# Performance work log

Hardware: AMD Instinct MI355X
Metric: run time of the kernel (lower is better)

Reference implementation:

```python
import jax, jax.numpy as jnp
import numpy as np

N, D = 8192, 256

def setup_inputs() -> dict:
    key = jax.random.key(0)
    k1, k2 = jax.random.split(key)
    data = jnp.zeros((1,), dtype=jnp.float32)  # unused by the module
    Z = jax.random.normal(k1, (N, D), dtype=jnp.float32)
    A_hat = jax.random.uniform(k2, (N, N), dtype=jnp.float32)
    return {"data": data, "Z": Z, "A_hat": A_hat}

def reference(data, Z, A_hat):
    A = A_hat.astype(jnp.float32)
    # D^{-1/2} A D^{-1/2}: diagonal matmuls are mathematically row/col scaling
    d_inv_sqrt = 1.0 / jnp.sqrt(A.sum(axis=1) + 1e-10)  # [N]
    A_norm = A * d_inv_sqrt[:, None] * d_inv_sqrt[None, :]  # [N, N]
    # cosine similarity (F.normalize uses eps=1e-12 clamp on the norm)
    z_norm = jnp.linalg.norm(Z, axis=1, keepdims=True)
    Z_n = Z / jnp.maximum(z_norm, 1e-12)
    similarity = Z_n @ Z_n.T  # [N, N]
    homo_loss = -jnp.sum(A_norm * similarity)
    hetero_loss = jnp.sum((1.0 - A_norm) * similarity)
    return (homo_loss, hetero_loss)
```

## Files before the change

kernel.cpp:

```cpp
#include <hip/hip_runtime.h>
#include <hip/hip_fp16.h>

typedef _Float16 f16x8  __attribute__((ext_vector_type(8)));
typedef _Float16 f16x4  __attribute__((ext_vector_type(4)));
typedef float    f32x16 __attribute__((ext_vector_type(16)));

constexpr int Nn = 8192;
constexpr int Dd = 256;

constexpr int BM  = 256;
constexpr int KC  = 1024;
constexpr int SK  = 16;
constexpr int NSC = KC / SK;
constexpr int NB  = 6;
constexpr int ABUF = BM * SK;
constexpr int YBUF = Dd * SK;

__global__ __launch_bounds__(256) void k_rowsum(const float* __restrict__ A,
                                                float* __restrict__ dis,
                                                float* __restrict__ rd,
                                                float* __restrict__ T) {
    if (blockIdx.x == 0 && threadIdx.x == 0) *T = 0.f;
    const int row  = blockIdx.x * 4 + (threadIdx.x >> 6);
    const int lane = threadIdx.x & 63;
    const float4* rp = reinterpret_cast<const float4*>(A + (size_t)row * Nn);
    float s = 0.f;
    #pragma unroll
    for (int i = 0; i < Nn / 256; ++i) {
        float4 v = rp[i * 64 + lane];
        s += (v.x + v.y) + (v.z + v.w);
    }
    #pragma unroll
    for (int off = 32; off > 0; off >>= 1) s += __shfl_down(s, off, 64);
    if (lane == 0) {
        float rs = s + 1e-10f;
        dis[row] = rsqrtf(rs);
        rd[row]  = sqrtf(rs);
    }
}

__global__ __launch_bounds__(256) void k_makeYt(const float* __restrict__ Z,
                                               const float* __restrict__ dis,
                                               _Float16* __restrict__ Yt,
                                               _Float16* __restrict__ Yr) {
    __shared__ float nrm[64][4];
    __shared__ _Float16 tile[Dd][72];
    const int t = threadIdx.x;
    const int r = t >> 2, q = t & 3;
    const int row = blockIdx.x * 64 + r;
    const float4* zp = reinterpret_cast<const float4*>(Z + (size_t)row * Dd + q * 64);
    float4 v[16];
    float ss = 0.f;
    #pragma unroll
    for (int i = 0; i < 16; ++i) {
        v[i] = zp[i];
        ss += v[i].x*v[i].x + v[i].y*v[i].y + v[i].z*v[i].z + v[i].w*v[i].w;
    }
    nrm[r][q] = ss;
    __syncthreads();
    const float tot   = nrm[r][0] + nrm[r][1] + nrm[r][2] + nrm[r][3];
    const float scale = dis[row] / fmaxf(sqrtf(tot), 1e-12f);
    #pragma unroll
    for (int i = 0; i < 16; ++i) {
        const int c0 = q * 64 + i * 4;
        f16x4 y = { (_Float16)(v[i].x * scale), (_Float16)(v[i].y * scale),
                    (_Float16)(v[i].z * scale), (_Float16)(v[i].w * scale) };
        tile[c0+0][r] = y[0];
        tile[c0+1][r] = y[1];
        tile[c0+2][r] = y[2];
        tile[c0+3][r] = y[3];
        *reinterpret_cast<f16x4*>(Yr + (size_t)row * Dd + c0) = y;
    }
    __syncthreads();
    int4*       dst = reinterpret_cast<int4*>(Yt + (size_t)t * Nn + blockIdx.x * 64);
    const int4* src = reinterpret_cast<const int4*>(&tile[t][0]);
    #pragma unroll
    for (int i = 0; i < 8; ++i) dst[i] = src[i];
}

__global__ __launch_bounds__(256) void k_colsum(const _Float16* __restrict__ Yt,
                                                const float* __restrict__ rd,
                                                float* __restrict__ s) {
    const int k = blockIdx.x;
    const int t = threadIdx.x;
    const _Float16* yp = Yt + (size_t)k * Nn + t * 32;
    const float*    rp = rd + t * 32;
    float acc = 0.f;
    #pragma unroll
    for (int i = 0; i < 32; ++i) acc += (float)yp[i] * rp[i];
    #pragma unroll
    for (int off = 32; off > 0; off >>= 1) acc += __shfl_down(acc, off, 64);
    __shared__ float red[4];
    if ((t & 63) == 0) red[t >> 6] = acc;
    __syncthreads();
    if (t == 0) s[k] = red[0] + red[1] + red[2] + red[3];
}

__global__ __launch_bounds__(1024, 4) void k_main(const float* __restrict__ A,
                                                  const _Float16* __restrict__ Yt,
                                                  const _Float16* __restrict__ Yr,
                                                  float* __restrict__ T) {
    __shared__ float    As[NB * ABUF];
    __shared__ _Float16 Ysm[NB * YBUF];

    const int ib = blockIdx.x & (Nn / BM - 1);
    const int jb = blockIdx.x >> 5;
    const int I0 = ib * BM;
    const int K0 = jb * KC;
    const int t   = threadIdx.x;
    const int w   = t >> 6;
    const int wm  = w >> 1;
    const int wn  = w & 1;
    const int l   = t & 63;
    const int ln  = l & 31;
    const int lkh = l >> 5;

    f32x16 acc[4];
    #pragma unroll
    for (int q = 0; q < 4; ++q) acc[q] = (f32x16)(0.f);

    #define STAGE(SC, B)                                                       \
    {   const int kc = K0 + (SC) * SK;                                         \
        {   const int rr = w * 16 + (l >> 2);                                  \
            const int sl = (l & 3) ^ ((l >> 3) & 3);                           \
            __builtin_amdgcn_global_load_lds(                                  \
                (const __attribute__((address_space(1))) unsigned int*)        \
                    (A + (size_t)(I0 + rr) * Nn + kc + sl * 4),                \
                (__attribute__((address_space(3))) unsigned int*)              \
                    (As + (B) * ABUF + w * 256),                               \
                16, 0, 0);                                                     \
        }                                                                      \
        if (w < 8) {                                                           \
            const int nr = w * 32 + (l >> 1);                                  \
            __builtin_amdgcn_global_load_lds(                                  \
                (const __attribute__((address_space(1))) unsigned int*)        \
                    (Yt + (size_t)nr * Nn + kc + (l & 1) * 8),                 \
                (__attribute__((address_space(3))) unsigned int*)              \
                    (Ysm + (B) * YBUF + w * 512),                              \
                16, 0, 0);                                                     \
        }                                                                      \
    }

    #define WAITV(N) asm volatile("s_waitcnt vmcnt(" #N ")" ::: "memory")

    STAGE(0, 0); STAGE(1, 1); STAGE(2, 2); STAGE(3, 3); STAGE(4, 4);

    for (int sc = 0; sc < NSC; ++sc) {
        const int ah = NSC - 1 - sc;
        if (w < 8) {
            if (ah >= 4) WAITV(8); else if (ah == 3) WAITV(6);
            else if (ah == 2) WAITV(4); else if (ah == 1) WAITV(2); else WAITV(0);
        } else {
            if (ah >= 4) WAITV(4); else if (ah == 3) WAITV(3);
            else if (ah == 2) WAITV(2); else if (ah == 1) WAITV(1); else WAITV(0);
        }
        __builtin_amdgcn_s_barrier();
        if (sc + 5 < NSC) STAGE(sc + 5, (sc + 5) % NB);

        const int cb = sc % NB;
        const float*    Ab = As  + cb * ABUF + (wm * 32 + ln) * SK;
        const _Float16* Yb = Ysm + cb * YBUF;
        const int q = (ln >> 1) & 3;
        const float4 u0 = *reinterpret_cast<const float4*>(Ab + ((lkh * 2)     ^ q) * 4);
        const float4 u1 = *reinterpret_cast<const float4*>(Ab + ((lkh * 2 + 1) ^ q) * 4);
        const f16x8 af = { (_Float16)u0.x, (_Float16)u0.y, (_Float16)u0.z, (_Float16)u0.w,
                           (_Float16)u1.x, (_Float16)u1.y, (_Float16)u1.z, (_Float16)u1.w };
        #pragma unroll
        for (int tn = 0; tn < 4; ++tn) {
            const int n = wn * 128 + tn * 32 + ln;
            const f16x8 bf = *reinterpret_cast<const f16x8*>(Yb + n * SK + lkh * 8);
            acc[tn] = __builtin_amdgcn_mfma_f32_32x32x16_f16(af, bf, acc[tn], 0, 0, 0);
        }
    }

    float part = 0.f;
    #pragma unroll
    for (int tn = 0; tn < 4; ++tn) {
        const int n = wn * 128 + tn * 32 + ln;
        #pragma unroll
        for (int r = 0; r < 16; ++r) {
            const int i = I0 + wm * 32 + (r & 3) + 8 * (r >> 2) + 4 * lkh;
            part += acc[tn][r] * (float)Yr[(size_t)i * Dd + n];
        }
    }
    #pragma unroll
    for (int off = 32; off > 0; off >>= 1) part += __shfl_down(part, off, 64);
    __shared__ float red[16];
    if (l == 0) red[w] = part;
    __syncthreads();
    if (threadIdx.x == 0) {
        float tt = 0.f;
        #pragma unroll
        for (int i = 0; i < 16; ++i) tt += red[i];
        atomicAdd(T, tt);
    }
}

__global__ __launch_bounds__(256) void k_final(const float* __restrict__ s,
                                               const float* __restrict__ T,
                                               float* __restrict__ out) {
    const int t = threadIdx.x;
    float v = s[t];
    float p = v * v;
    #pragma unroll
    for (int off = 32; off > 0; off >>= 1) p += __shfl_down(p, off, 64);
    __shared__ float red[4];
    if ((t & 63) == 0) red[t >> 6] = p;
    __syncthreads();
    if (t == 0) {
        const float ss = red[0] + red[1] + red[2] + red[3];
        const float Tv = *T;
        out[0] = -Tv;
        out[1] = ss - Tv;
    }
}

extern "C" void kernel_launch(void* const* d_in, const int* in_sizes, int n_in,
                              void* d_out, int out_size, void* d_ws, size_t ws_size,
                              hipStream_t stream) {
    const float* Z = (const float*)d_in[1];
    const float* A = (const float*)d_in[2];
    float* out = (float*)d_out;

    char* ws = (char*)d_ws;
    float*    dis = (float*)(ws);
    float*    rd  = (float*)(ws + 32768);
    float*    s   = (float*)(ws + 65536);
    float*    T   = (float*)(ws + 66560);
    _Float16* Yt  = (_Float16*)(ws + 131072);
    _Float16* Yr  = (_Float16*)(ws + 131072 + (size_t)Nn * Dd * 2);

    k_rowsum<<<Nn / 4, 256, 0, stream>>>(A, dis, rd, T);
    k_makeYt<<<Nn / 64, 256, 0, stream>>>(Z, dis, Yt, Yr);
    k_colsum<<<Dd, 256, 0, stream>>>(Yt, rd, s);
    k_main<<<(Nn / BM) * (Nn / KC), 1024, 0, stream>>>(A, Yt, Yr, T);
    k_final<<<1, 256, 0, stream>>>(s, T, out);
}
```

Baseline: 142.9 us.

## Convert A and Yt to FP8 and use fp8 MFMA in main kernel

The row-sum pass now also writes an FP8 copy of A, and the projected features are stored transposed in FP8, scaled by 64 to stay in FP8 range. The main kernel streams 1-byte operands with a larger K step and four buffers, and uses the 32x32x16 fp8 MFMA; the result is rescaled by 1/64 at the end. This aims to cut the main kernel's memory traffic and conversion work. The cost is an extra 64MB write in the row pass and reduced precision of A and Y, which may hurt accuracy. The column-sum kernel is also rewritten to read the row-major fp16 features with atomics.

Result: faster. 126.9 us, median of 2 (-11.2%).

```diff
diff --git a/kernel.cpp b/kernel.cpp
--- a/kernel.cpp
+++ b/kernel.cpp
@@ -1,7 +1,6 @@
 #include <hip/hip_runtime.h>
 #include <hip/hip_fp16.h>
 
-typedef _Float16 f16x8  __attribute__((ext_vector_type(8)));
 typedef _Float16 f16x4  __attribute__((ext_vector_type(4)));
 typedef float    f32x16 __attribute__((ext_vector_type(16)));
 
@@ -10,30 +9,42 @@
 
 constexpr int BM  = 256;
 constexpr int KC  = 1024;
-constexpr int SK  = 16;
+constexpr int SK  = 64;
 constexpr int NSC = KC / SK;
-constexpr int NB  = 6;
-constexpr int ABUF = BM * SK;
-constexpr int YBUF = Dd * SK;
-
-__global__ __launch_bounds__(256) void k_rowsum(const float* __restrict__ A,
+constexpr int NB  = 4;
+constexpr int ABYTES = BM * SK;
+constexpr int YBYTES = Dd * SK;
+
+#define AS1 __attribute__((address_space(1)))
+#define AS3 __attribute__((address_space(3)))
+
+__global__ __launch_bounds__(256) void k_rowcvt(const float* __restrict__ A,
+                                                unsigned char* __restrict__ Af8,
                                                 float* __restrict__ dis,
                                                 float* __restrict__ rd,
+                                                float* __restrict__ s,
                                                 float* __restrict__ T) {
-    if (blockIdx.x == 0 && threadIdx.x == 0) *T = 0.f;
+    if (blockIdx.x == 0) {
+        if (threadIdx.x == 0) *T = 0.f;
+        s[threadIdx.x] = 0.f;
+    }
     const int row  = blockIdx.x * 4 + (threadIdx.x >> 6);
     const int lane = threadIdx.x & 63;
-    const float4* rp = reinterpret_cast<const float4*>(A + (size_t)row * Nn);
-    float s = 0.f;
+    const float4*  rp = reinterpret_cast<const float4*>(A + (size_t)row * Nn);
+    unsigned int*  wp = reinterpret_cast<unsigned int*>(Af8 + (size_t)row * Nn);
+    float sum = 0.f;
     #pragma unroll
     for (int i = 0; i < Nn / 256; ++i) {
         float4 v = rp[i * 64 + lane];
-        s += (v.x + v.y) + (v.z + v.w);
-    }
-    #pragma unroll
-    for (int off = 32; off > 0; off >>= 1) s += __shfl_down(s, off, 64);
+        sum += (v.x + v.y) + (v.z + v.w);
+        int p = __builtin_amdgcn_cvt_pk_fp8_f32(v.x, v.y, 0, false);
+        p     = __builtin_amdgcn_cvt_pk_fp8_f32(v.z, v.w, p, true);
+        wp[i * 64 + lane] = (unsigned int)p;
+    }
+    #pragma unroll
+    for (int off = 32; off > 0; off >>= 1) sum += __shfl_down(sum, off, 64);
     if (lane == 0) {
-        float rs = s + 1e-10f;
+        float rs = sum + 1e-10f;
         dis[row] = rsqrtf(rs);
         rd[row]  = sqrtf(rs);
     }
@@ -41,10 +52,10 @@
 
 __global__ __launch_bounds__(256) void k_makeYt(const float* __restrict__ Z,
                                                const float* __restrict__ dis,
-                                               _Float16* __restrict__ Yt,
+                                               unsigned char* __restrict__ Ytf8,
                                                _Float16* __restrict__ Yr) {
     __shared__ float nrm[64][4];
-    __shared__ _Float16 tile[Dd][72];
+    __shared__ unsigned char tile[Dd][80];
     const int t = threadIdx.x;
     const int r = t >> 2, q = t & 3;
     const int row = blockIdx.x * 64 + r;
@@ -58,50 +69,49 @@
     }
     nrm[r][q] = ss;
     __syncthreads();
-    const float tot   = nrm[r][0] + nrm[r][1] + nrm[r][2] + nrm[r][3];
-    const float scale = dis[row] / fmaxf(sqrtf(tot), 1e-12f);
+    const float tot  = nrm[r][0] + nrm[r][1] + nrm[r][2] + nrm[r][3];
+    const float sc   = dis[row] / fmaxf(sqrtf(tot), 1e-12f);
+    const float sc8  = 64.f * sc;
     #pragma unroll
     for (int i = 0; i < 16; ++i) {
         const int c0 = q * 64 + i * 4;
-        f16x4 y = { (_Float16)(v[i].x * scale), (_Float16)(v[i].y * scale),
-                    (_Float16)(v[i].z * scale), (_Float16)(v[i].w * scale) };
-        tile[c0+0][r] = y[0];
-        tile[c0+1][r] = y[1];
-        tile[c0+2][r] = y[2];
-        tile[c0+3][r] = y[3];
+        f16x4 y = { (_Float16)(v[i].x * sc), (_Float16)(v[i].y * sc),
+                    (_Float16)(v[i].z * sc), (_Float16)(v[i].w * sc) };
         *reinterpret_cast<f16x4*>(Yr + (size_t)row * Dd + c0) = y;
-    }
-    __syncthreads();
-    int4*       dst = reinterpret_cast<int4*>(Yt + (size_t)t * Nn + blockIdx.x * 64);
+        int p = __builtin_amdgcn_cvt_pk_fp8_f32(v[i].x * sc8, v[i].y * sc8, 0, false);
+        p     = __builtin_amdgcn_cvt_pk_fp8_f32(v[i].z * sc8, v[i].w * sc8, p, true);
+        tile[c0+0][r] = (unsigned char)(p);
+        tile[c0+1][r] = (unsigned char)(p >> 8);
+        tile[c0+2][r] = (unsigned char)(p >> 16);
+        tile[c0+3][r] = (unsigned char)(p >> 24);
+    }
+    __syncthreads();
+    int4*       dst = reinterpret_cast<int4*>(Ytf8 + (size_t)t * Nn + blockIdx.x * 64);
     const int4* src = reinterpret_cast<const int4*>(&tile[t][0]);
     #pragma unroll
-    for (int i = 0; i < 8; ++i) dst[i] = src[i];
-}
-
-__global__ __launch_bounds__(256) void k_colsum(const _Float16* __restrict__ Yt,
+    for (int i = 0; i < 4; ++i) dst[i] = src[i];
+}
+
+__global__ __launch_bounds__(256) void k_colsum(const _Float16* __restrict__ Yr,
                                                 const float* __restrict__ rd,
                                                 float* __restrict__ s) {
-    const int k = blockIdx.x;
-    const int t = threadIdx.x;
-    const _Float16* yp = Yt + (size_t)k * Nn + t * 32;
-    const float*    rp = rd + t * 32;
+    const int c  = threadIdx.x;
+    const int r0 = blockIdx.x * 256;
     float acc = 0.f;
-    #pragma unroll
-    for (int i = 0; i < 32; ++i) acc += (float)yp[i] * rp[i];
-    #pragma unroll
-    for (int off = 32; off > 0; off >>= 1) acc += __shfl_down(acc, off, 64);
-    __shared__ float red[4];
-    if ((t & 63) == 0) red[t >> 6] = acc;
-    __syncthreads();
-    if (t == 0) s[k] = red[0] + red[1] + red[2] + red[3];
-}
-
-__global__ __launch_bounds__(1024, 4) void k_main(const float* __restrict__ A,
-                                                  const _Float16* __restrict__ Yt,
+    const _Float16* yp = Yr + (size_t)r0 * Dd + c;
+    #pragma unroll 8
+    for (int r = 0; r < 256; ++r) acc += (float)yp[(size_t)r * Dd] * rd[r0 + r];
+    atomicAdd(&s[c], acc);
+}
+
+__global__ __launch_bounds__(1024, 4) void k_main(const unsigned char* __restrict__ Af8,
+                                                  const unsigned char* __restrict__ Ytf8,
                                                   const _Float16* __restrict__ Yr,
                                                   float* __restrict__ T) {
-    __shared__ float    As[NB * ABUF];
-    __shared__ _Float16 Ysm[NB * YBUF];
+    __shared__ long As[NB * ABYTES / 8];
+    __shared__ long Ys[NB * YBYTES / 8];
+    char* As8 = (char*)As;
+    char* Ys8 = (char*)Ys;
 
     const int ib = blockIdx.x & (Nn / BM - 1);
     const int jb = blockIdx.x >> 5;
@@ -121,55 +131,43 @@
 
     #define STAGE(SC, B)                                                       \
     {   const int kc = K0 + (SC) * SK;                                         \
-        {   const int rr = w * 16 + (l >> 2);                                  \
-            const int sl = (l & 3) ^ ((l >> 3) & 3);                           \
-            __builtin_amdgcn_global_load_lds(                                  \
-                (const __attribute__((address_space(1))) unsigned int*)        \
-                    (A + (size_t)(I0 + rr) * Nn + kc + sl * 4),                \
-                (__attribute__((address_space(3))) unsigned int*)              \
-                    (As + (B) * ABUF + w * 256),                               \
-                16, 0, 0);                                                     \
-        }                                                                      \
-        if (w < 8) {                                                           \
-            const int nr = w * 32 + (l >> 1);                                  \
-            __builtin_amdgcn_global_load_lds(                                  \
-                (const __attribute__((address_space(1))) unsigned int*)        \
-                    (Yt + (size_t)nr * Nn + kc + (l & 1) * 8),                 \
-                (__attribute__((address_space(3))) unsigned int*)              \
-                    (Ysm + (B) * YBUF + w * 512),                              \
-                16, 0, 0);                                                     \
-        }                                                                      \
+        const int rr = w * 16 + (l >> 2);                                      \
+        const int sg = ((l & 3) ^ ((rr >> 1) & 3)) * 16;                       \
+        __builtin_amdgcn_global_load_lds(                                      \
+            (const AS1 unsigned int*)(Af8 + (size_t)(I0 + rr) * Nn + kc + sg), \
+            (AS3 unsigned int*)(As8 + (B) * ABYTES + w * 1024), 16, 0, 0);     \
+        __builtin_amdgcn_global_load_lds(                                      \
+            (const AS1 unsigned int*)(Ytf8 + (size_t)rr * Nn + kc + sg),       \
+            (AS3 unsigned int*)(Ys8 + (B) * YBYTES + w * 1024), 16, 0, 0);     \
     }
 
     #define WAITV(N) asm volatile("s_waitcnt vmcnt(" #N ")" ::: "memory")
 
-    STAGE(0, 0); STAGE(1, 1); STAGE(2, 2); STAGE(3, 3); STAGE(4, 4);
+    STAGE(0, 0); STAGE(1, 1); STAGE(2, 2);
 
     for (int sc = 0; sc < NSC; ++sc) {
         const int ah = NSC - 1 - sc;
-        if (w < 8) {
-            if (ah >= 4) WAITV(8); else if (ah == 3) WAITV(6);
-            else if (ah == 2) WAITV(4); else if (ah == 1) WAITV(2); else WAITV(0);
-        } else {
-            if (ah >= 4) WAITV(4); else if (ah == 3) WAITV(3);
-            else if (ah == 2) WAITV(2); else if (ah == 1) WAITV(1); else WAITV(0);
-        }
+        if (ah >= 2) WAITV(4); else if (ah == 1) WAITV(2); else WAITV(0);
         __builtin_amdgcn_s_barrier();
-        if (sc + 5 < NSC) STAGE(sc + 5, (sc + 5) % NB);
-
-        const int cb = sc % NB;
-        const float*    Ab = As  + cb * ABUF + (wm * 32 + ln) * SK;
-        const _Float16* Yb = Ysm + cb * YBUF;
-        const int q = (ln >> 1) & 3;
-        const float4 u0 = *reinterpret_cast<const float4*>(Ab + ((lkh * 2)     ^ q) * 4);
-        const float4 u1 = *reinterpret_cast<const float4*>(Ab + ((lkh * 2 + 1) ^ q) * 4);
-        const f16x8 af = { (_Float16)u0.x, (_Float16)u0.y, (_Float16)u0.z, (_Float16)u0.w,
-                           (_Float16)u1.x, (_Float16)u1.y, (_Float16)u1.z, (_Float16)u1.w };
+        if (sc + 3 < NSC) STAGE(sc + 3, (sc + 3) & 3);
+
+        const int cb = sc & 3;
+        const long* Al = reinterpret_cast<const long*>(As8 + cb * ABYTES);
+        const long* Yl = reinterpret_cast<const long*>(Ys8 + cb * YBYTES);
+        const int r  = wm * 32 + ln;
+        const int xA = ((r >> 1) & 3) << 1;
+        long af[4];
+        #pragma unroll
+        for (int ks = 0; ks < 4; ++ks) af[ks] = Al[r * 8 + ((ks * 2 + lkh) ^ xA)];
         #pragma unroll
         for (int tn = 0; tn < 4; ++tn) {
-            const int n = wn * 128 + tn * 32 + ln;
-            const f16x8 bf = *reinterpret_cast<const f16x8*>(Yb + n * SK + lkh * 8);
-            acc[tn] = __builtin_amdgcn_mfma_f32_32x32x16_f16(af, bf, acc[tn], 0, 0, 0);
+            const int n  = wn * 128 + tn * 32 + ln;
+            const int xN = ((n >> 1) & 3) << 1;
+            #pragma unroll
+            for (int ks = 0; ks < 4; ++ks) {
+                const long bf = Yl[n * 8 + ((ks * 2 + lkh) ^ xN)];
+                acc[tn] = __builtin_amdgcn_mfma_f32_32x32x16_fp8_fp8(af[ks], bf, acc[tn], 0, 0, 0);
+            }
         }
     }
 
@@ -178,9 +176,9 @@
     for (int tn = 0; tn < 4; ++tn) {
         const int n = wn * 128 + tn * 32 + ln;
         #pragma unroll
-        for (int r = 0; r < 16; ++r) {
-            const int i = I0 + wm * 32 + (r & 3) + 8 * (r >> 2) + 4 * lkh;
-            part += acc[tn][r] * (float)Yr[(size_t)i * Dd + n];
+        for (int rr = 0; rr < 16; ++rr) {
+            const int i = I0 + wm * 32 + (rr & 3) + 8 * (rr >> 2) + 4 * lkh;
+            part += acc[tn][rr] * (float)Yr[(size_t)i * Dd + n];
         }
     }
     #pragma unroll
@@ -192,7 +190,7 @@
         float tt = 0.f;
         #pragma unroll
         for (int i = 0; i < 16; ++i) tt += red[i];
-        atomicAdd(T, tt);
+        atomicAdd(T, tt * 0.015625f);
     }
 }
 
@@ -223,16 +221,17 @@
     float* out = (float*)d_out;
 
     char* ws = (char*)d_ws;
-    float*    dis = (float*)(ws);
-    float*    rd  = (float*)(ws + 32768);
-    float*    s   = (float*)(ws + 65536);
-    float*    T   = (float*)(ws + 66560);
-    _Float16* Yt  = (_Float16*)(ws + 131072);
-    _Float16* Yr  = (_Float16*)(ws + 131072 + (size_t)Nn * Dd * 2);
-
-    k_rowsum<<<Nn / 4, 256, 0, stream>>>(A, dis, rd, T);
-    k_makeYt<<<Nn / 64, 256, 0, stream>>>(Z, dis, Yt, Yr);
-    k_colsum<<<Dd, 256, 0, stream>>>(Yt, rd, s);
-    k_main<<<(Nn / BM) * (Nn / KC), 1024, 0, stream>>>(A, Yt, Yr, T);
+    float*         dis  = (float*)(ws);
+    float*         rd   = (float*)(ws + 32768);
+    float*         s    = (float*)(ws + 65536);
+    float*         T    = (float*)(ws + 66560);
+    _Float16*      Yr   = (_Float16*)(ws + 131072);
+    unsigned char* Ytf8 = (unsigned char*)(ws + 131072 + (size_t)Nn * Dd * 2);
+    unsigned char* Af8  = (unsigned char*)(ws + 131072 + (size_t)Nn * Dd * 3);
+
+    k_rowcvt<<<Nn / 4, 256, 0, stream>>>(A, Af8, dis, rd, s, T);
+    k_makeYt<<<Nn / 64, 256, 0, stream>>>(Z, dis, Ytf8, Yr);
+    k_colsum<<<Nn / 256, 256, 0, stream>>>(Yr, rd, s);
+    k_main<<<(Nn / BM) * (Nn / KC), 1024, 0, stream>>>(Af8, Ytf8, Yr, T);
     k_final<<<1, 256, 0, stream>>>(s, T, out);
 }
```
